# Optimization experiments

Hardware: AMD Instinct MI355X
Metric: run time of the kernel (lower is better)

Reference implementation:

```python
import jax, jax.numpy as jnp
import numpy as np

WIN = 5  # half-window of the 11x11 exclusion zone around the peak
EPS = 1e-5


def setup_inputs() -> dict:
    key = jax.random.key(0)
    # B is hard-coded to 8 in the original module (mean/std buffers of size 8); C must be 1
    response = jax.random.normal(key, (8, 1, 2048, 2048), dtype=jnp.float32)
    return {"response": response}


def reference(response):
    B, C, H, W = response.shape
    flat = response.reshape(B, -1)                      # [B, H*W] (C == 1)
    idx = jnp.argmax(flat, axis=1)
    cy = idx // W                                       # [B]
    cx = idx % W                                        # [B]

    rows = jnp.arange(H)
    cols = jnp.arange(W)
    # 11x11 window around peak; clamping via max/min in the original is equivalent
    # to these open-range comparisons.
    in_y = (rows[None, :] >= cy[:, None] - WIN) & (rows[None, :] < cy[:, None] + WIN + 1)  # [B,H]
    in_x = (cols[None, :] >= cx[:, None] - WIN) & (cols[None, :] < cx[:, None] + WIN + 1)  # [B,W]
    window = in_y[:, None, :, None] & in_x[:, None, None, :]                               # [B,1,H,W]

    masked = jnp.where(window, jnp.zeros((), response.dtype), response)  # response * mask
    pos = masked > 0                                    # data-dependent sidelobe selection

    n = jnp.sum(pos, axis=(1, 2, 3)).astype(response.dtype)             # [B]
    s = jnp.sum(jnp.where(pos, masked, 0.0), axis=(1, 2, 3))            # [B]
    mean = s / n                                                         # [B]
    dev2 = jnp.where(pos, (masked - mean[:, None, None, None]) ** 2, 0.0)
    # torch.std defaults to unbiased (ddof=1)
    std = jnp.sqrt(jnp.sum(dev2, axis=(1, 2, 3)) / (n - 1.0))           # [B]

    f_max = jnp.max(flat, axis=1)                                        # [B]
    psr = (f_max - mean) / (std + EPS)
    return jnp.mean(psr)
```

## Files before the change

### kernel.cpp

```cpp
#include <hip/hip_runtime.h>
#include <math.h>

constexpr int HH   = 2048;
constexpr int WW   = 2048;
constexpr int BB   = 8;
constexpr unsigned NPB  = (unsigned)HH * (unsigned)WW;
constexpr unsigned NVEC = NPB / 4;
constexpr int NBLK = 256;
constexpr int TPB  = 256;
constexpr int WIN  = 5;

__device__ __forceinline__ void argmax_combine(float& bv, unsigned& bi,
                                               float ov, unsigned oi) {
    if (ov > bv || (ov == bv && oi < bi)) { bv = ov; bi = oi; }
}

__global__ __launch_bounds__(TPB) void psr_pass1(
    const float* __restrict__ resp,
    double* __restrict__ dS, double* __restrict__ dSS,
    float* __restrict__ fM, unsigned* __restrict__ uI,
    unsigned* __restrict__ uC)
{
    const int b = blockIdx.y;
    const float4* __restrict__ base =
        reinterpret_cast<const float4*>(resp) + (size_t)b * NVEC;
    const unsigned tid = blockIdx.x * TPB + threadIdx.x;

    float fsum = 0.f, fss = 0.f;
    float bv = -INFINITY;
    unsigned bi = 0, cnt = 0;

    #pragma unroll 4
    for (unsigned v = tid; v < NVEC; v += (unsigned)(NBLK * TPB)) {
        float4 x = base[v];
        unsigned e0 = v * 4u;
        float r;
        r = fmaxf(x.x, 0.f); fsum += r; fss = fmaf(r, r, fss); cnt += (x.x > 0.f);
        if (x.x > bv) { bv = x.x; bi = e0; }
        r = fmaxf(x.y, 0.f); fsum += r; fss = fmaf(r, r, fss); cnt += (x.y > 0.f);
        if (x.y > bv) { bv = x.y; bi = e0 + 1u; }
        r = fmaxf(x.z, 0.f); fsum += r; fss = fmaf(r, r, fss); cnt += (x.z > 0.f);
        if (x.z > bv) { bv = x.z; bi = e0 + 2u; }
        r = fmaxf(x.w, 0.f); fsum += r; fss = fmaf(r, r, fss); cnt += (x.w > 0.f);
        if (x.w > bv) { bv = x.w; bi = e0 + 3u; }
    }

    double ds = (double)fsum, dss = (double)fss;
    for (int off = 32; off > 0; off >>= 1) {
        ds  += __shfl_down(ds,  off, 64);
        dss += __shfl_down(dss, off, 64);
        cnt += __shfl_down(cnt, off, 64);
        float    ov = __shfl_down(bv, off, 64);
        unsigned oi = __shfl_down(bi, off, 64);
        argmax_combine(bv, bi, ov, oi);
    }

    __shared__ double sds[4], sdss[4];
    __shared__ float  sbv[4];
    __shared__ unsigned sbi[4], scnt[4];
    const int wave = threadIdx.x >> 6;
    const int lane = threadIdx.x & 63;
    if (lane == 0) {
        sds[wave] = ds; sdss[wave] = dss;
        sbv[wave] = bv; sbi[wave] = bi; scnt[wave] = cnt;
    }
    __syncthreads();
    if (threadIdx.x == 0) {
        for (int w = 1; w < 4; ++w) {
            ds += sds[w]; dss += sdss[w]; cnt += scnt[w];
            argmax_combine(bv, bi, sbv[w], sbi[w]);
        }
        const unsigned p = (unsigned)b * NBLK + blockIdx.x;
        dS[p] = ds; dSS[p] = dss; fM[p] = bv; uI[p] = bi; uC[p] = cnt;
    }
}

__global__ __launch_bounds__(TPB) void psr_pass2(
    const float* __restrict__ resp,
    const double* __restrict__ dS, const double* __restrict__ dSS,
    const float* __restrict__ fM, const unsigned* __restrict__ uI,
    const unsigned* __restrict__ uC,
    float* __restrict__ psr)
{
    const int b = blockIdx.x;
    const int t = threadIdx.x;
    const unsigned p = (unsigned)b * NBLK + (unsigned)t;

    double ds = dS[p], dss = dSS[p];
    float bv = fM[p];
    unsigned bi = uI[p], cnt = uC[p];

    for (int off = 32; off > 0; off >>= 1) {
        ds  += __shfl_down(ds,  off, 64);
        dss += __shfl_down(dss, off, 64);
        cnt += __shfl_down(cnt, off, 64);
        float    ov = __shfl_down(bv, off, 64);
        unsigned oi = __shfl_down(bi, off, 64);
        argmax_combine(bv, bi, ov, oi);
    }

    __shared__ double sds[4], sdss[4];
    __shared__ float  sbv[4];
    __shared__ unsigned sbi[4], scnt[4];
    const int wave = t >> 6;
    const int lane = t & 63;
    if (lane == 0) {
        sds[wave] = ds; sdss[wave] = dss;
        sbv[wave] = bv; sbi[wave] = bi; scnt[wave] = cnt;
    }
    __syncthreads();

    __shared__ double gS, gSS;
    __shared__ float  gM;
    __shared__ unsigned gI, gC;
    if (t == 0) {
        for (int w = 1; w < 4; ++w) {
            ds += sds[w]; dss += sdss[w]; cnt += scnt[w];
            argmax_combine(bv, bi, sbv[w], sbi[w]);
        }
        gS = ds; gSS = dss; gM = bv; gI = bi; gC = cnt;
    }
    __syncthreads();

    const unsigned idx = gI;
    const int cy = (int)(idx >> 11);
    const int cx = (int)(idx & 2047u);

    double wsum = 0.0, wss = 0.0;
    unsigned wcnt = 0;
    if (t < (2 * WIN + 1) * (2 * WIN + 1)) {
        const int dy = t / 11 - WIN;
        const int dx = t % 11 - WIN;
        const int y = cy + dy, x = cx + dx;
        if (y >= 0 && y < HH && x >= 0 && x < WW) {
            const float v = resp[(size_t)b * NPB + (size_t)y * WW + (size_t)x];
            if (v > 0.f) { wsum = (double)v; wss = (double)v * (double)v; wcnt = 1; }
        }
    }
    for (int off = 32; off > 0; off >>= 1) {
        wsum += __shfl_down(wsum, off, 64);
        wss  += __shfl_down(wss,  off, 64);
        wcnt += __shfl_down(wcnt, off, 64);
    }
    __shared__ double wds[4], wdss[4];
    __shared__ unsigned wdc[4];
    if (lane == 0) { wds[wave] = wsum; wdss[wave] = wss; wdc[wave] = wcnt; }
    __syncthreads();

    if (t == 0) {
        for (int w = 1; w < 4; ++w) { wsum += wds[w]; wss += wdss[w]; wcnt += wdc[w]; }
        const double S  = gS  - wsum;
        const double SS = gSS - wss;
        const double N  = (double)(gC - wcnt);
        const double mean = S / N;
        const double var  = (SS - N * mean * mean) / (N - 1.0);
        const double sd   = sqrt(var);
        psr[b] = (float)(((double)gM - mean) / (sd + 1e-5));
    }
}

__global__ void psr_pass3(const float* __restrict__ psr, float* __restrict__ out) {
    const int t = threadIdx.x;
    float v = (t < BB) ? psr[t] : 0.f;
    v += __shfl_down(v, 4, 64);
    v += __shfl_down(v, 2, 64);
    v += __shfl_down(v, 1, 64);
    if (t == 0) out[0] = v * (1.0f / BB);
}

extern "C" void kernel_launch(void* const* d_in, const int* in_sizes, int n_in,
                              void* d_out, int out_size, void* d_ws, size_t ws_size,
                              hipStream_t stream) {
    const float* resp = (const float*)d_in[0];
    float* out = (float*)d_out;

    char* ws = (char*)d_ws;
    double*   dS  = (double*)(ws);
    double*   dSS = (double*)(ws + 16384);
    float*    fM  = (float*)(ws + 32768);
    unsigned* uI  = (unsigned*)(ws + 40960);
    unsigned* uC  = (unsigned*)(ws + 49152);
    float*    psr = (float*)(ws + 57344);

    dim3 g1(NBLK, BB);
    psr_pass1<<<g1, TPB, 0, stream>>>(resp, dS, dSS, fM, uI, uC);
    psr_pass2<<<BB, TPB, 0, stream>>>(resp, dS, dSS, fM, uI, uC, psr);
    psr_pass3<<<1, 64, 0, stream>>>(psr, out);
}
```

Baseline: 190.5 us.

## Fully unroll streaming loop, ballot-based counting, and fuse finalize kernels

The pass-1 loop is fully unrolled with a compile-time trip count. The positive count now uses wave ballot plus popcount instead of per-lane increments, and the argmax first takes a 4-wide max before any compare and branch. Pass 2 and pass 3 are merged into one single-block kernel in which each wave handles two batches, which removes a launch. All of this cuts ALU work in a bandwidth-bound 128 MB scan and trims tail latency. The trade-off is higher register pressure from full unrolling and a serial finalize on one block.

New measurement: 199.7 us. 4.9% more time.

```diff
diff --git a/kernel.cpp b/kernel.cpp
--- a/kernel.cpp
+++ b/kernel.cpp
@@ -8,7 +8,8 @@
 constexpr unsigned NVEC = NPB / 4;
 constexpr int NBLK = 256;
 constexpr int TPB  = 256;
-constexpr int WIN  = 5;
+constexpr unsigned STRIDE = (unsigned)(NBLK * TPB);
+constexpr int NITER = (int)(NVEC / STRIDE);
 
 __device__ __forceinline__ void argmax_combine(float& bv, unsigned& bi,
                                                float ov, unsigned oi) {
@@ -28,28 +29,42 @@
 
     float fsum = 0.f, fss = 0.f;
     float bv = -INFINITY;
-    unsigned bi = 0, cnt = 0;
+    unsigned bi = 0;
+    unsigned long long cnt = 0;
 
-    #pragma unroll 4
-    for (unsigned v = tid; v < NVEC; v += (unsigned)(NBLK * TPB)) {
+    #pragma unroll
+    for (int i = 0; i < NITER; ++i) {
+        const unsigned v = tid + (unsigned)i * STRIDE;
         float4 x = base[v];
-        unsigned e0 = v * 4u;
+
         float r;
-        r = fmaxf(x.x, 0.f); fsum += r; fss = fmaf(r, r, fss); cnt += (x.x > 0.f);
-        if (x.x > bv) { bv = x.x; bi = e0; }
-        r = fmaxf(x.y, 0.f); fsum += r; fss = fmaf(r, r, fss); cnt += (x.y > 0.f);
-        if (x.y > bv) { bv = x.y; bi = e0 + 1u; }
-        r = fmaxf(x.z, 0.f); fsum += r; fss = fmaf(r, r, fss); cnt += (x.z > 0.f);
-        if (x.z > bv) { bv = x.z; bi = e0 + 2u; }
-        r = fmaxf(x.w, 0.f); fsum += r; fss = fmaf(r, r, fss); cnt += (x.w > 0.f);
-        if (x.w > bv) { bv = x.w; bi = e0 + 3u; }
+        r = fmaxf(x.x, 0.f); fsum += r; fss = fmaf(r, r, fss);
+        r = fmaxf(x.y, 0.f); fsum += r; fss = fmaf(r, r, fss);
+        r = fmaxf(x.z, 0.f); fsum += r; fss = fmaf(r, r, fss);
+        r = fmaxf(x.w, 0.f); fsum += r; fss = fmaf(r, r, fss);
+
+        cnt += __popcll(__ballot(x.x > 0.f));
+        cnt += __popcll(__ballot(x.y > 0.f));
+        cnt += __popcll(__ballot(x.z > 0.f));
+        cnt += __popcll(__ballot(x.w > 0.f));
+
+        const float m01 = fmaxf(x.x, x.y);
+        const float m23 = fmaxf(x.z, x.w);
+        const float m4  = fmaxf(m01, m23);
+        if (m4 > bv) {
+            bv = m4;
+            const unsigned e0 = v * 4u;
+            bi = (x.x == m4) ? e0
+               : (x.y == m4) ? e0 + 1u
+               : (x.z == m4) ? e0 + 2u
+               : e0 + 3u;
+        }
     }
 
     double ds = (double)fsum, dss = (double)fss;
     for (int off = 32; off > 0; off >>= 1) {
         ds  += __shfl_down(ds,  off, 64);
         dss += __shfl_down(dss, off, 64);
-        cnt += __shfl_down(cnt, off, 64);
         float    ov = __shfl_down(bv, off, 64);
         unsigned oi = __shfl_down(bi, off, 64);
         argmax_combine(bv, bi, ov, oi);
@@ -62,16 +77,17 @@
     const int lane = threadIdx.x & 63;
     if (lane == 0) {
         sds[wave] = ds; sdss[wave] = dss;
-        sbv[wave] = bv; sbi[wave] = bi; scnt[wave] = cnt;
+        sbv[wave] = bv; sbi[wave] = bi; scnt[wave] = (unsigned)cnt;
     }
     __syncthreads();
     if (threadIdx.x == 0) {
+        unsigned ctot = scnt[0];
         for (int w = 1; w < 4; ++w) {
-            ds += sds[w]; dss += sdss[w]; cnt += scnt[w];
+            ds += sds[w]; dss += sdss[w]; ctot += scnt[w];
             argmax_combine(bv, bi, sbv[w], sbi[w]);
         }
         const unsigned p = (unsigned)b * NBLK + blockIdx.x;
-        dS[p] = ds; dSS[p] = dss; fM[p] = bv; uI[p] = bi; uC[p] = cnt;
+        dS[p] = ds; dSS[p] = dss; fM[p] = bv; uI[p] = bi; uC[p] = ctot;
     }
 }
 
@@ -80,92 +96,74 @@
     const double* __restrict__ dS, const double* __restrict__ dSS,
     const float* __restrict__ fM, const unsigned* __restrict__ uI,
     const unsigned* __restrict__ uC,
-    float* __restrict__ psr)
+    float* __restrict__ out)
 {
-    const int b = blockIdx.x;
     const int t = threadIdx.x;
-    const unsigned p = (unsigned)b * NBLK + (unsigned)t;
-
-    double ds = dS[p], dss = dSS[p];
-    float bv = fM[p];
-    unsigned bi = uI[p], cnt = uC[p];
-
-    for (int off = 32; off > 0; off >>= 1) {
-        ds  += __shfl_down(ds,  off, 64);
-        dss += __shfl_down(dss, off, 64);
-        cnt += __shfl_down(cnt, off, 64);
-        float    ov = __shfl_down(bv, off, 64);
-        unsigned oi = __shfl_down(bi, off, 64);
-        argmax_combine(bv, bi, ov, oi);
-    }
-
-    __shared__ double sds[4], sdss[4];
-    __shared__ float  sbv[4];
-    __shared__ unsigned sbi[4], scnt[4];
     const int wave = t >> 6;
     const int lane = t & 63;
-    if (lane == 0) {
-        sds[wave] = ds; sdss[wave] = dss;
-        sbv[wave] = bv; sbi[wave] = bi; scnt[wave] = cnt;
+    __shared__ double s_psr[BB];
+
+    for (int rep = 0; rep < 2; ++rep) {
+        const int b = wave + rep * 4;
+
+        double ds = 0.0, dss = 0.0, dcnt = 0.0;
+        float bv = -INFINITY;
+        unsigned bi = 0xFFFFFFFFu;
+        #pragma unroll
+        for (int c = 0; c < NBLK / 64; ++c) {
+            const unsigned p = (unsigned)b * NBLK + (unsigned)(c * 64 + lane);
+            ds   += dS[p];
+            dss  += dSS[p];
+            dcnt += (double)uC[p];
+            argmax_combine(bv, bi, fM[p], uI[p]);
+        }
+        for (int off = 32; off > 0; off >>= 1) {
+            ds   += __shfl_down(ds,   off, 64);
+            dss  += __shfl_down(dss,  off, 64);
+            dcnt += __shfl_down(dcnt, off, 64);
+            float    ov = __shfl_down(bv, off, 64);
+            unsigned oi = __shfl_down(bi, off, 64);
+            argmax_combine(bv, bi, ov, oi);
+        }
+        const unsigned idx = (unsigned)__shfl((int)bi, 0, 64);
+        const int cy = (int)(idx >> 11);
+        const int cx = (int)(idx & 2047u);
+
+        double wsum = 0.0, wss = 0.0, wcnt = 0.0;
+        for (int k = lane; k < 121; k += 64) {
+            const int dy = k / 11 - 5;
+            const int dx = k % 11 - 5;
+            const int y = cy + dy, x = cx + dx;
+            if (y >= 0 && y < HH && x >= 0 && x < WW) {
+                const float v = resp[(size_t)b * NPB + (size_t)y * WW + (size_t)x];
+                if (v > 0.f) {
+                    wsum += (double)v;
+                    wss  += (double)v * (double)v;
+                    wcnt += 1.0;
+                }
+            }
+        }
+        for (int off = 32; off > 0; off >>= 1) {
+            wsum += __shfl_down(wsum, off, 64);
+            wss  += __shfl_down(wss,  off, 64);
+            wcnt += __shfl_down(wcnt, off, 64);
+        }
+
+        if (lane == 0) {
+            const double S  = ds  - wsum;
+            const double SS = dss - wss;
+            const double N  = dcnt - wcnt;
+            const double mean = S / N;
+            const double var  = (SS - N * mean * mean) / (N - 1.0);
+            s_psr[b] = ((double)bv - mean) / (sqrt(var) + 1e-5);
+        }
     }
     __syncthreads();
-
-    __shared__ double gS, gSS;
-    __shared__ float  gM;
-    __shared__ unsigned gI, gC;
     if (t == 0) {
-        for (int w = 1; w < 4; ++w) {
-            ds += sds[w]; dss += sdss[w]; cnt += scnt[w];
-            argmax_combine(bv, bi, sbv[w], sbi[w]);
-        }
-        gS = ds; gSS = dss; gM = bv; gI = bi; gC = cnt;
+        double a = 0.0;
+        for (int b2 = 0; b2 < BB; ++b2) a += s_psr[b2];
+        out[0] = (float)(a / BB);
     }
-    __syncthreads();
-
-    const unsigned idx = gI;
-    const int cy = (int)(idx >> 11);
-    const int cx = (int)(idx & 2047u);
-
-    double wsum = 0.0, wss = 0.0;
-    unsigned wcnt = 0;
-    if (t < (2 * WIN + 1) * (2 * WIN + 1)) {
-        const int dy = t / 11 - WIN;
-        const int dx = t % 11 - WIN;
-        const int y = cy + dy, x = cx + dx;
-        if (y >= 0 && y < HH && x >= 0 && x < WW) {
-            const float v = resp[(size_t)b * NPB + (size_t)y * WW + (size_t)x];
-            if (v > 0.f) { wsum = (double)v; wss = (double)v * (double)v; wcnt = 1; }
-        }
-    }
-    for (int off = 32; off > 0; off >>= 1) {
-        wsum += __shfl_down(wsum, off, 64);
-        wss  += __shfl_down(wss,  off, 64);
-        wcnt += __shfl_down(wcnt, off, 64);
-    }
-    __shared__ double wds[4], wdss[4];
-    __shared__ unsigned wdc[4];
-    if (lane == 0) { wds[wave] = wsum; wdss[wave] = wss; wdc[wave] = wcnt; }
-    __syncthreads();
-
-    if (t == 0) {
-        for (int w = 1; w < 4; ++w) { wsum += wds[w]; wss += wdss[w]; wcnt += wdc[w]; }
-        const double S  = gS  - wsum;
-        const double SS = gSS - wss;
-        const double N  = (double)(gC - wcnt);
-        const double mean = S / N;
-        const double var  = (SS - N * mean * mean) / (N - 1.0);
-        const double sd   = sqrt(var);
-        psr[b] = (float)(((double)gM - mean) / (sd + 1e-5));
-    }
-}
-
-__global__ void psr_pass3(const float* __restrict__ psr, float* __restrict__ out) {
-    const int t = threadIdx.x;
-    float v = (t < BB) ? psr[t] : 0.f;
-    v += __shfl_down(v, 4, 64);
-    v += __shfl_down(v, 2, 64);
-    v += __shfl_down(v, 1, 64);
-    if (t == 0) out[0] = v * (1.0f / BB);
 }
 
 extern "C" void kernel_launch(void* const* d_in, const int* in_sizes, int n_in,
@@ -180,10 +178,8 @@
     float*    fM  = (float*)(ws + 32768);
     unsigned* uI  = (unsigned*)(ws + 40960);
     unsigned* uC  = (unsigned*)(ws + 49152);
-    float*    psr = (float*)(ws + 57344);
 
     dim3 g1(NBLK, BB);
     psr_pass1<<<g1, TPB, 0, stream>>>(resp, dS, dSS, fM, uI, uC);
-    psr_pass2<<<BB, TPB, 0, stream>>>(resp, dS, dSS, fM, uI, uC, psr);
-    psr_pass3<<<1, 64, 0, stream>>>(psr, out);
+    psr_pass2<<<1, TPB, 0, stream>>>(resp, dS, dSS, fM, uI, uC, out);
 }
```
